# Kernel optimization log

Hardware: AMD Instinct MI355X
Metric: run time of the kernel (lower is better)

Reference implementation:

```python
import jax, jax.numpy as jnp
import numpy as np


def setup_inputs() -> dict:
    key = jax.random.key(0)
    ks = jax.random.split(key, 7)
    B, F, D = 1024, 32, 64
    H = [128, 128, 128]
    x = jax.random.normal(ks[0], (B, F, D), dtype=jnp.float32)
    # Conv1d(k=1) weights: (out, in) where in = prev_field * F, Kaiming-ish scale
    W0 = jax.random.normal(ks[1], (H[0], F * F), dtype=jnp.float32) * 0.02
    b0 = jnp.zeros((H[0],), dtype=jnp.float32)
    W1 = jax.random.normal(ks[2], (H[1], H[0] * F), dtype=jnp.float32) * 0.02
    b1 = jnp.zeros((H[1],), dtype=jnp.float32)
    W2 = jax.random.normal(ks[3], (H[2], H[1] * F), dtype=jnp.float32) * 0.02
    b2 = jnp.zeros((H[2],), dtype=jnp.float32)
    return {"x": x, "W0": W0, "b0": b0, "W1": W1, "b1": b1, "W2": W2, "b2": b2}


def reference(x, W0, b0, W1, b1, W2, b2):
    # CIN: per layer, outer product of current hidden with base fields along
    # embed dim, then 1x1 conv (channel mix) + ReLU. We fuse the bhmd
    # intermediate directly into the contraction: W reshaped to (o, h, m)
    # matches torch's reshape(b, h*m, d) channel ordering (h major, m minor).
    F = x.shape[1]
    x0 = x  # (b, m=F, d)
    h = x
    res = []
    for W, b in ((W0, b0), (W1, b1), (W2, b2)):
        o = W.shape[0]
        Wr = W.reshape(o, h.shape[1], F)  # (o, h, m)
        z = jnp.einsum('bhd,bmd,ohm->bod', h, x0, Wr) + b[None, :, None]
        h = jax.nn.relu(z)
        res.append(h)
    out = jnp.concatenate(res, axis=1)  # (b, sum(H), d)
    return jnp.sum(out, axis=-1)  # (b, sum(H))
```

## Files before the change

### kernel.cpp

```cpp
#include <hip/hip_runtime.h>
#include <stdint.h>


typedef __attribute__((ext_vector_type(8))) _Float16 f16x8;
typedef __attribute__((ext_vector_type(4))) float f32x4;
typedef __attribute__((ext_vector_type(4))) int i32x4;

union AB {
  i32x4 i;
  f16x8 h;
  uint32_t u[4];
};

static __device__ __forceinline__ uint16_t f_to_f16u(float a) {
  return __builtin_bit_cast(uint16_t, (_Float16)a);
}
static __device__ __forceinline__ uint32_t dup16(uint16_t u) {
  return (uint32_t)u | ((uint32_t)u << 16);
}

#define HP 132

__global__ __launch_bounds__(256, 4) void cin_main(
    const float* __restrict__ x, const uint16_t* __restrict__ wp,
    const float* __restrict__ bias0, const float* __restrict__ bias1,
    const float* __restrict__ bias2, float* __restrict__ out) {
  __shared__ __align__(16) uint32_t hD[64][HP];

  const int tid = threadIdx.x;
  const int w = tid >> 6, lane = tid & 63;
  const int q = lane >> 4, i = lane & 15;
  const int b = blockIdx.x;

  for (int e = tid; e < 2048; e += 256) {
    int m = e >> 6, d = e & 63;
    hD[d][m] = dup16(f_to_f16u(x[(size_t)b * 2048 + e]));
  }
  __syncthreads();

  AB xf[4];
#pragma unroll
  for (int t = 0; t < 4; ++t) {
    const uint32_t* p = &hD[t * 16 + i][q * 8];
    uint4 r0 = *(const uint4*)p;
    uint4 r1 = *(const uint4*)(p + 4);
    xf[t].u[0] = __builtin_amdgcn_perm(r0.y, r0.x, 0x05040100u);
    xf[t].u[1] = __builtin_amdgcn_perm(r0.w, r0.z, 0x05040100u);
    xf[t].u[2] = __builtin_amdgcn_perm(r1.y, r1.x, 0x05040100u);
    xf[t].u[3] = __builtin_amdgcn_perm(r1.w, r1.z, 0x05040100u);
  }

#pragma unroll
  for (int L = 0; L < 3; ++L) {
    const int Kch = (L == 0) ? 32 : 128;
    const uint16_t* W = (L == 0) ? wp : (L == 1) ? wp + 131072 : wp + 131072 + 524288;
    const float* bias = (L == 0) ? bias0 : (L == 1) ? bias1 : bias2;

    const uint16_t* wB0 = W + ((size_t)(2 * w) * Kch) * 512 + lane * 8;
    const uint16_t* wB1 = W + ((size_t)(2 * w + 1) * Kch) * 512 + lane * 8;

    f32x4 acc[4][2];
#pragma unroll
    for (int t = 0; t < 4; ++t)
#pragma unroll
      for (int g = 0; g < 2; ++g) acc[t][g] = (f32x4){0.f, 0.f, 0.f, 0.f};

    AB a0[2], a1[2];
    a0[0].i = *(const i32x4*)(wB0);
    a0[1].i = *(const i32x4*)(wB1);

#pragma unroll 1
    for (int c0 = 0; c0 < Kch; c0 += 2) {
      a1[0].i = *(const i32x4*)(wB0 + (size_t)(c0 + 1) * 512);
      a1[1].i = *(const i32x4*)(wB1 + (size_t)(c0 + 1) * 512);

      uint2 hv[4];
#pragma unroll
      for (int t = 0; t < 4; ++t) hv[t] = *(const uint2*)&hD[t * 16 + i][c0];

#pragma unroll
      for (int t = 0; t < 4; ++t) {
        AB hs, bf;
        hs.u[0] = hv[t].x; hs.u[1] = hv[t].x; hs.u[2] = hv[t].x; hs.u[3] = hv[t].x;
        bf.h = hs.h * xf[t].h;
        acc[t][0] = __builtin_amdgcn_mfma_f32_16x16x32_f16(a0[0].h, bf.h, acc[t][0], 0, 0, 0);
        acc[t][1] = __builtin_amdgcn_mfma_f32_16x16x32_f16(a0[1].h, bf.h, acc[t][1], 0, 0, 0);
      }

      int cn = (c0 + 2 < Kch) ? c0 + 2 : 0;
      a0[0].i = *(const i32x4*)(wB0 + (size_t)cn * 512);
      a0[1].i = *(const i32x4*)(wB1 + (size_t)cn * 512);

#pragma unroll
      for (int t = 0; t < 4; ++t) {
        AB hs, bf;
        hs.u[0] = hv[t].y; hs.u[1] = hv[t].y; hs.u[2] = hv[t].y; hs.u[3] = hv[t].y;
        bf.h = hs.h * xf[t].h;
        acc[t][0] = __builtin_amdgcn_mfma_f32_16x16x32_f16(a1[0].h, bf.h, acc[t][0], 0, 0, 0);
        acc[t][1] = __builtin_amdgcn_mfma_f32_16x16x32_f16(a1[1].h, bf.h, acc[t][1], 0, 0, 0);
      }
    }

    f32x4 bv[2];
    bv[0] = *(const f32x4*)(bias + (2 * w) * 16 + q * 4);
    bv[1] = *(const f32x4*)(bias + (2 * w + 1) * 16 + q * 4);
#pragma unroll
    for (int t = 0; t < 4; ++t)
#pragma unroll
      for (int g = 0; g < 2; ++g)
#pragma unroll
        for (int r = 0; r < 4; ++r)
          acc[t][g][r] = fmaxf(acc[t][g][r] + bv[g][r], 0.f);

    if (L < 2) {
      __syncthreads();
#pragma unroll
      for (int t = 0; t < 4; ++t)
#pragma unroll
        for (int g = 0; g < 2; ++g) {
          uint4 pk;
          pk.x = dup16(f_to_f16u(acc[t][g][0]));
          pk.y = dup16(f_to_f16u(acc[t][g][1]));
          pk.z = dup16(f_to_f16u(acc[t][g][2]));
          pk.w = dup16(f_to_f16u(acc[t][g][3]));
          *(uint4*)&hD[t * 16 + i][(2 * w + g) * 16 + q * 4] = pk;
        }
      __syncthreads();
    }

#pragma unroll
    for (int g = 0; g < 2; ++g)
#pragma unroll
      for (int r = 0; r < 4; ++r) {
        float s = acc[0][g][r] + acc[1][g][r] + acc[2][g][r] + acc[3][g][r];
        s += __shfl_xor(s, 1);
        s += __shfl_xor(s, 2);
        s += __shfl_xor(s, 4);
        s += __shfl_xor(s, 8);
        if (i == 0)
          out[(size_t)b * 384 + L * 128 + (2 * w + g) * 16 + q * 4 + r] = s;
      }
  }
}

__global__ void pack_w(const float* __restrict__ W, uint16_t* __restrict__ Wp,
                       int kshift) {
  const int Kch = 1 << kshift;
  int idx = blockIdx.x * 256 + threadIdx.x;
  int lane = idx & 63;
  int qq = lane >> 4, ii = lane & 15;
  int rest = idx >> 6;
  int c = rest & (Kch - 1);
  int ot = rest >> kshift;
  const float* src = W + (size_t)(ot * 16 + ii) * (Kch * 32) + c * 32 + qq * 8;
  uint32_t o[4];
#pragma unroll
  for (int k = 0; k < 4; ++k)
    o[k] = (uint32_t)f_to_f16u(src[2 * k]) | ((uint32_t)f_to_f16u(src[2 * k + 1]) << 16);
  uint4 val;
  val.x = o[0]; val.y = o[1]; val.z = o[2]; val.w = o[3];
  *(uint4*)(Wp + (size_t)idx * 8) = val;
}

extern "C" void kernel_launch(void* const* d_in, const int* in_sizes, int n_in,
                              void* d_out, int out_size, void* d_ws, size_t ws_size,
                              hipStream_t stream) {
  (void)in_sizes; (void)n_in; (void)out_size; (void)ws_size;
  const float* x  = (const float*)d_in[0];
  const float* W0 = (const float*)d_in[1];
  const float* b0 = (const float*)d_in[2];
  const float* W1 = (const float*)d_in[3];
  const float* b1 = (const float*)d_in[4];
  const float* W2 = (const float*)d_in[5];
  const float* b2 = (const float*)d_in[6];
  uint16_t* wpacked = (uint16_t*)d_ws;

  hipLaunchKernelGGL(pack_w, dim3(64),  dim3(256), 0, stream, W0, wpacked, 5);
  hipLaunchKernelGGL(pack_w, dim3(256), dim3(256), 0, stream, W1, wpacked + 131072, 7);
  hipLaunchKernelGGL(pack_w, dim3(256), dim3(256), 0, stream, W2, wpacked + 131072 + 524288, 7);
  hipLaunchKernelGGL(cin_main, dim3(1024), dim3(256), 0, stream,
                     x, wpacked, b0, b1, b2, (float*)d_out);
}
```

Baseline: 203.3 us.

## Switch to 32x32x16 MFMA with two batches per 512-thread block

Restructures the CIN kernel so each block processes two batch rows with 8 waves, using 32x32x16 f16 MFMA tiles instead of 16x16x32. Hidden state is stored as packed f16 (no duplicated halves), and the B operand is built with packed f16 multiplies against broadcast hidden values. Weights are double-buffered across two channel pairs and repacked for the new tile layout, and row sums go through shared memory before being written out. The aim is fewer, larger MFMA instructions, less LDS traffic, and weight loads shared across two batches. The cost is a new reduction path and an extra barrier per layer.

```diff
diff --git a/kernel.cpp b/kernel.cpp
--- a/kernel.cpp
+++ b/kernel.cpp
@@ -3,6 +3,8 @@
 
 
 typedef __attribute__((ext_vector_type(8))) _Float16 f16x8;
+typedef __attribute__((ext_vector_type(2))) _Float16 f16x2;
+typedef __attribute__((ext_vector_type(16))) float f32x16;
 typedef __attribute__((ext_vector_type(4))) float f32x4;
 typedef __attribute__((ext_vector_type(4))) int i32x4;
 
@@ -12,134 +14,145 @@
   uint32_t u[4];
 };
 
-static __device__ __forceinline__ uint16_t f_to_f16u(float a) {
-  return __builtin_bit_cast(uint16_t, (_Float16)a);
+static __device__ __forceinline__ uint32_t pkmul(uint32_t a, uint32_t b) {
+  f16x2 r = __builtin_bit_cast(f16x2, a) * __builtin_bit_cast(f16x2, b);
+  return __builtin_bit_cast(uint32_t, r);
 }
-static __device__ __forceinline__ uint32_t dup16(uint16_t u) {
-  return (uint32_t)u | ((uint32_t)u << 16);
+static __device__ __forceinline__ uint32_t pkcvt(float a, float b) {
+  return __builtin_bit_cast(uint32_t, __builtin_amdgcn_cvt_pkrtz(a, b));
 }
 
-#define HP 132
+#define HP 136
 
-__global__ __launch_bounds__(256, 4) void cin_main(
+__global__ __launch_bounds__(512, 4) void cin_main(
     const float* __restrict__ x, const uint16_t* __restrict__ wp,
     const float* __restrict__ bias0, const float* __restrict__ bias1,
     const float* __restrict__ bias2, float* __restrict__ out) {
-  __shared__ __align__(16) uint32_t hD[64][HP];
+  __shared__ __align__(16) uint16_t hT[2][64][HP];
+  __shared__ float sOut[2][2][128];
 
   const int tid = threadIdx.x;
   const int w = tid >> 6, lane = tid & 63;
-  const int q = lane >> 4, i = lane & 15;
-  const int b = blockIdx.x;
+  const int p = w >> 2;
+  const int nt = (w >> 1) & 1;
+  const int og = w & 1;
+  const int l5 = lane >> 5, l31 = lane & 31;
+  const int dd = nt * 32 + l31;
+  const int bb = blockIdx.x * 2;
 
-  for (int e = tid; e < 2048; e += 256) {
-    int m = e >> 6, d = e & 63;
-    hD[d][m] = dup16(f_to_f16u(x[(size_t)b * 2048 + e]));
+  for (int e = tid; e < 4096; e += 512) {
+    int p2 = e >> 11, m = (e >> 6) & 31, d = e & 63;
+    hT[p2][d][m] =
+        __builtin_bit_cast(uint16_t, (_Float16)x[(size_t)(bb + p2) * 2048 + m * 64 + d]);
   }
   __syncthreads();
 
-  AB xf[4];
+  AB xf[2];
 #pragma unroll
-  for (int t = 0; t < 4; ++t) {
-    const uint32_t* p = &hD[t * 16 + i][q * 8];
-    uint4 r0 = *(const uint4*)p;
-    uint4 r1 = *(const uint4*)(p + 4);
-    xf[t].u[0] = __builtin_amdgcn_perm(r0.y, r0.x, 0x05040100u);
-    xf[t].u[1] = __builtin_amdgcn_perm(r0.w, r0.z, 0x05040100u);
-    xf[t].u[2] = __builtin_amdgcn_perm(r1.y, r1.x, 0x05040100u);
-    xf[t].u[3] = __builtin_amdgcn_perm(r1.w, r1.z, 0x05040100u);
-  }
+  for (int kh = 0; kh < 2; ++kh)
+    xf[kh].i = *(const i32x4*)&hT[p][dd][kh * 16 + l5 * 8];
+
+  f32x16 acc[2];
 
 #pragma unroll
   for (int L = 0; L < 3; ++L) {
     const int Kch = (L == 0) ? 32 : 128;
-    const uint16_t* W = (L == 0) ? wp : (L == 1) ? wp + 131072 : wp + 131072 + 524288;
+    const uint16_t* wl = (L == 0) ? wp : (L == 1) ? wp + 131072 : wp + 655360;
     const float* bias = (L == 0) ? bias0 : (L == 1) ? bias1 : bias2;
 
-    const uint16_t* wB0 = W + ((size_t)(2 * w) * Kch) * 512 + lane * 8;
-    const uint16_t* wB1 = W + ((size_t)(2 * w + 1) * Kch) * 512 + lane * 8;
-
-    f32x4 acc[4][2];
-#pragma unroll
-    for (int t = 0; t < 4; ++t)
-#pragma unroll
-      for (int g = 0; g < 2; ++g) acc[t][g] = (f32x4){0.f, 0.f, 0.f, 0.f};
-
-    AB a0[2], a1[2];
-    a0[0].i = *(const i32x4*)(wB0);
-    a0[1].i = *(const i32x4*)(wB1);
-
-#pragma unroll 1
-    for (int c0 = 0; c0 < Kch; c0 += 2) {
-      a1[0].i = *(const i32x4*)(wB0 + (size_t)(c0 + 1) * 512);
-      a1[1].i = *(const i32x4*)(wB1 + (size_t)(c0 + 1) * 512);
-
-      uint2 hv[4];
-#pragma unroll
-      for (int t = 0; t < 4; ++t) hv[t] = *(const uint2*)&hD[t * 16 + i][c0];
+    const uint16_t* wptr[2];
+    wptr[0] = wl + (size_t)(og * 2 + 0) * Kch * 1024 + lane * 8;
+    wptr[1] = wl + (size_t)(og * 2 + 1) * Kch * 1024 + lane * 8;
 
 #pragma unroll
-      for (int t = 0; t < 4; ++t) {
-        AB hs, bf;
-        hs.u[0] = hv[t].x; hs.u[1] = hv[t].x; hs.u[2] = hv[t].x; hs.u[3] = hv[t].x;
-        bf.h = hs.h * xf[t].h;
-        acc[t][0] = __builtin_amdgcn_mfma_f32_16x16x32_f16(a0[0].h, bf.h, acc[t][0], 0, 0, 0);
-        acc[t][1] = __builtin_amdgcn_mfma_f32_16x16x32_f16(a0[1].h, bf.h, acc[t][1], 0, 0, 0);
-      }
+    for (int g = 0; g < 2; ++g)
+#pragma unroll
+      for (int r = 0; r < 16; ++r) acc[g][r] = 0.f;
 
-      int cn = (c0 + 2 < Kch) ? c0 + 2 : 0;
-      a0[0].i = *(const i32x4*)(wB0 + (size_t)cn * 512);
-      a0[1].i = *(const i32x4*)(wB1 + (size_t)cn * 512);
+    AB bufA[2][2][2], bufB[2][2][2];
 
+    auto loadW = [&](AB (&buf)[2][2][2], int c) {
 #pragma unroll
-      for (int t = 0; t < 4; ++t) {
-        AB hs, bf;
-        hs.u[0] = hv[t].y; hs.u[1] = hv[t].y; hs.u[2] = hv[t].y; hs.u[3] = hv[t].y;
-        bf.h = hs.h * xf[t].h;
-        acc[t][0] = __builtin_amdgcn_mfma_f32_16x16x32_f16(a1[0].h, bf.h, acc[t][0], 0, 0, 0);
-        acc[t][1] = __builtin_amdgcn_mfma_f32_16x16x32_f16(a1[1].h, bf.h, acc[t][1], 0, 0, 0);
-      }
-    }
-
-    f32x4 bv[2];
-    bv[0] = *(const f32x4*)(bias + (2 * w) * 16 + q * 4);
-    bv[1] = *(const f32x4*)(bias + (2 * w + 1) * 16 + q * 4);
+      for (int cc = 0; cc < 2; ++cc)
 #pragma unroll
-    for (int t = 0; t < 4; ++t)
+        for (int g = 0; g < 2; ++g)
 #pragma unroll
-      for (int g = 0; g < 2; ++g)
+          for (int kh = 0; kh < 2; ++kh)
+            buf[cc][g][kh].i =
+                *(const i32x4*)(wptr[g] + (size_t)(c + cc) * 1024 + kh * 512);
+    };
+    auto compute2 = [&](int c0, AB (&buf)[2][2][2]) {
+      uint32_t hv = *(const uint32_t*)&hT[p][dd][c0];
 #pragma unroll
-        for (int r = 0; r < 4; ++r)
-          acc[t][g][r] = fmaxf(acc[t][g][r] + bv[g][r], 0.f);
-
-    if (L < 2) {
-      __syncthreads();
+      for (int cc = 0; cc < 2; ++cc) {
+        uint32_t hd = __builtin_amdgcn_perm(hv, hv, cc ? 0x03020302u : 0x01000100u);
+        AB bf0, bf1;
 #pragma unroll
-      for (int t = 0; t < 4; ++t)
+        for (int k = 0; k < 4; ++k) {
+          bf0.u[k] = pkmul(hd, xf[0].u[k]);
+          bf1.u[k] = pkmul(hd, xf[1].u[k]);
+        }
 #pragma unroll
         for (int g = 0; g < 2; ++g) {
-          uint4 pk;
-          pk.x = dup16(f_to_f16u(acc[t][g][0]));
-          pk.y = dup16(f_to_f16u(acc[t][g][1]));
-          pk.z = dup16(f_to_f16u(acc[t][g][2]));
-          pk.w = dup16(f_to_f16u(acc[t][g][3]));
-          *(uint4*)&hD[t * 16 + i][(2 * w + g) * 16 + q * 4] = pk;
+          acc[g] = __builtin_amdgcn_mfma_f32_32x32x16_f16(buf[cc][g][0].h, bf0.h, acc[g], 0, 0, 0);
+          acc[g] = __builtin_amdgcn_mfma_f32_32x32x16_f16(buf[cc][g][1].h, bf1.h, acc[g], 0, 0, 0);
         }
-      __syncthreads();
+      }
+    };
+
+    loadW(bufA, 0);
+#pragma unroll 1
+    for (int c0 = 0; c0 < Kch; c0 += 4) {
+      loadW(bufB, c0 + 2);
+      compute2(c0, bufA);
+      loadW(bufA, (c0 + 4 < Kch) ? c0 + 4 : 0);
+      compute2(c0 + 2, bufB);
     }
 
 #pragma unroll
     for (int g = 0; g < 2; ++g)
 #pragma unroll
-      for (int r = 0; r < 4; ++r) {
-        float s = acc[0][g][r] + acc[1][g][r] + acc[2][g][r] + acc[3][g][r];
+      for (int q4 = 0; q4 < 4; ++q4) {
+        f32x4 bv = *(const f32x4*)(bias + (og * 2 + g) * 32 + 8 * q4 + 4 * l5);
+#pragma unroll
+        for (int r = 0; r < 4; ++r)
+          acc[g][q4 * 4 + r] = fmaxf(acc[g][q4 * 4 + r] + bv[r], 0.f);
+      }
+
+#pragma unroll
+    for (int g = 0; g < 2; ++g)
+#pragma unroll
+      for (int r = 0; r < 16; ++r) {
+        float s = acc[g][r];
         s += __shfl_xor(s, 1);
         s += __shfl_xor(s, 2);
         s += __shfl_xor(s, 4);
         s += __shfl_xor(s, 8);
-        if (i == 0)
-          out[(size_t)b * 384 + L * 128 + (2 * w + g) * 16 + q * 4 + r] = s;
+        s += __shfl_xor(s, 16);
+        if (l31 == 0)
+          sOut[p][nt][(og * 2 + g) * 32 + (r & 3) + 8 * (r >> 2) + 4 * l5] = s;
       }
+
+    __syncthreads();
+
+    if (L < 2) {
+#pragma unroll
+      for (int g = 0; g < 2; ++g)
+#pragma unroll
+        for (int q4 = 0; q4 < 4; ++q4) {
+          uint2 pk;
+          pk.x = pkcvt(acc[g][q4 * 4 + 0], acc[g][q4 * 4 + 1]);
+          pk.y = pkcvt(acc[g][q4 * 4 + 2], acc[g][q4 * 4 + 3]);
+          *(uint2*)&hT[p][dd][(og * 2 + g) * 32 + 8 * q4 + 4 * l5] = pk;
+        }
+    }
+
+    if (tid < 256) {
+      int b2 = tid >> 7, o = tid & 127;
+      out[(size_t)(bb + b2) * 384 + L * 128 + o] = sOut[b2][0][o] + sOut[b2][1][o];
+    }
+
+    if (L < 2) __syncthreads();
   }
 }
 
@@ -148,17 +161,16 @@
   const int Kch = 1 << kshift;
   int idx = blockIdx.x * 256 + threadIdx.x;
   int lane = idx & 63;
-  int qq = lane >> 4, ii = lane & 15;
-  int rest = idx >> 6;
-  int c = rest & (Kch - 1);
-  int ot = rest >> kshift;
-  const float* src = W + (size_t)(ot * 16 + ii) * (Kch * 32) + c * 32 + qq * 8;
-  uint32_t o[4];
-#pragma unroll
-  for (int k = 0; k < 4; ++k)
-    o[k] = (uint32_t)f_to_f16u(src[2 * k]) | ((uint32_t)f_to_f16u(src[2 * k + 1]) << 16);
+  int kh = (idx >> 6) & 1;
+  int c = (idx >> 7) & (Kch - 1);
+  int ot = idx >> (7 + kshift);
+  const float* src = W + (size_t)(ot * 32 + (lane & 31)) * (Kch * 32) +
+                     c * 32 + kh * 16 + (lane >> 5) * 8;
   uint4 val;
-  val.x = o[0]; val.y = o[1]; val.z = o[2]; val.w = o[3];
+  val.x = pkcvt(src[0], src[1]);
+  val.y = pkcvt(src[2], src[3]);
+  val.z = pkcvt(src[4], src[5]);
+  val.w = pkcvt(src[6], src[7]);
   *(uint4*)(Wp + (size_t)idx * 8) = val;
 }
 
@@ -177,7 +189,7 @@
 
   hipLaunchKernelGGL(pack_w, dim3(64),  dim3(256), 0, stream, W0, wpacked, 5);
   hipLaunchKernelGGL(pack_w, dim3(256), dim3(256), 0, stream, W1, wpacked + 131072, 7);
-  hipLaunchKernelGGL(pack_w, dim3(256), dim3(256), 0, stream, W2, wpacked + 131072 + 524288, 7);
-  hipLaunchKernelGGL(cin_main, dim3(1024), dim3(256), 0, stream,
+  hipLaunchKernelGGL(pack_w, dim3(256), dim3(256), 0, stream, W2, wpacked + 655360, 7);
+  hipLaunchKernelGGL(cin_main, dim3(512), dim3(512), 0, stream,
                      x, wpacked, b0, b1, b2, (float*)d_out);
 }
```

Result: slower. 299.1 us (+47.1%).
